# Kernel optimization log

Hardware: AMD Instinct MI355X
Metric: run time of the kernel (lower is better)

Reference implementation:

```python
import jax, jax.numpy as jnp
import numpy as np

N_NODES = 100000
N_EDGES = 1600000
D_IN = 128
D_HID = 128
GARMENT_SIZE = 80000


def setup_inputs() -> dict:
    key = jax.random.key(0)
    k1, k2, k3, k4, k5, k6 = jax.random.split(key, 6)
    notes = jax.random.normal(k1, (N_NODES, D_IN), dtype=jnp.float32)
    w = jax.random.normal(k2, (D_IN, D_HID), dtype=jnp.float32) * 0.05
    b = jax.random.normal(k3, (D_HID,), dtype=jnp.float32) * 0.05
    edge_src = jax.random.randint(k4, (N_EDGES,), 0, N_NODES, dtype=jnp.int32)
    edge_dst = jax.random.randint(k5, (N_EDGES,), 0, N_NODES, dtype=jnp.int32)
    edge_w = jax.random.uniform(k6, (N_EDGES,), dtype=jnp.float32)
    return {
        "notes": notes,
        "w": w,
        "b": b,
        "edge_src": edge_src,
        "edge_dst": edge_dst,
        "edge_w": edge_w,
        "garment_size": GARMENT_SIZE,
    }


def reference(notes, w, b, edge_src, edge_dst, edge_w, garment_size):
    # Dense projection: X0 = notes @ w   -> [N, H]
    X0 = jnp.einsum("nd,dh->nh", notes, w)
    # edge_convolution_template(edge_function=lambda x, y: y, reduction='weighted'):
    # X1[i] = sum over edges (i -> j) of a_ij * X0[j]
    msgs = X0[edge_dst] * edge_w[:, None]                      # [E, H] gather + scale
    X1 = jax.ops.segment_sum(msgs, edge_src, num_segments=notes.shape[0])  # [N, H]
    X = X1 + b
    # concat(act(X), X0[garment_size:]) along node axis -> [2N - garment_size, H]
    return jnp.concatenate([jax.nn.relu(X), X0[garment_size:]], axis=0)
```

## Files before the change

### kernel.cpp

```cpp
#include <hip/hip_runtime.h>

#define H 128
#define NPB 128
#define NB_MAX 1024
#define FILL_CH 4096
#define BCAP 3072
#define GCAP 2560

static __device__ __forceinline__ unsigned short f2bf(float f) {
  unsigned u = __float_as_uint(f);
  u += 0x7FFFu + ((u >> 16) & 1u);
  return (unsigned short)(u >> 16);
}

__global__ __launch_bounds__(256) void gemm_kernel(
    const float* __restrict__ notes, const float* __restrict__ w,
    const int* __restrict__ g_ptr, unsigned short* __restrict__ x0h,
    float* __restrict__ out, int* __restrict__ cursor, int nb,
    int n_nodes) {
  __shared__ float wtile[32 * H];
  __shared__ float ntile[64 * 32];
  const int tid = threadIdx.x;

  if (blockIdx.x == 0) {
    for (int i = tid; i < nb; i += 256) cursor[i] = i * BCAP;
  }

  const int tx = tid & 31;
  const int ty = tid >> 5;
  const int rowBlk = blockIdx.x * 64;
  const int g = *g_ptr;

  float acc[8][4];
#pragma unroll
  for (int i = 0; i < 8; ++i)
#pragma unroll
    for (int j = 0; j < 4; ++j) acc[i][j] = 0.f;

  for (int kc = 0; kc < H; kc += 32) {
    __syncthreads();
    {
      const float4* wg = (const float4*)(w + (size_t)kc * H);
      float4* wl = (float4*)wtile;
#pragma unroll
      for (int i = 0; i < 4; ++i) wl[tid + i * 256] = wg[tid + i * 256];
    }
    {
      float4* nl = (float4*)ntile;
#pragma unroll
      for (int i = 0; i < 2; ++i) {
        const int idx = tid + i * 256;
        const int row = idx >> 3;
        const int q = idx & 7;
        const int rr = min(rowBlk + row, n_nodes - 1);
        nl[idx] = *(const float4*)(notes + (size_t)rr * H + kc + q * 4);
      }
    }
    __syncthreads();
#pragma unroll 8
    for (int kk = 0; kk < 32; ++kk) {
      const float4 b4 = *(const float4*)&wtile[kk * H + tx * 4];
      float a[8];
#pragma unroll
      for (int i = 0; i < 8; ++i) a[i] = ntile[(ty * 8 + i) * 32 + kk];
#pragma unroll
      for (int i = 0; i < 8; ++i) {
        acc[i][0] += a[i] * b4.x;
        acc[i][1] += a[i] * b4.y;
        acc[i][2] += a[i] * b4.z;
        acc[i][3] += a[i] * b4.w;
      }
    }
  }

#pragma unroll
  for (int i = 0; i < 8; ++i) {
    const int r = rowBlk + ty * 8 + i;
    if (r < n_nodes) {
      ushort4 h;
      h.x = f2bf(acc[i][0]);
      h.y = f2bf(acc[i][1]);
      h.z = f2bf(acc[i][2]);
      h.w = f2bf(acc[i][3]);
      *(ushort4*)(x0h + (size_t)r * H + tx * 4) = h;
      if (r >= g) {
        float4 v;
        v.x = acc[i][0]; v.y = acc[i][1]; v.z = acc[i][2]; v.w = acc[i][3];
        *(float4*)(out + (size_t)(n_nodes + r - g) * H + tx * 4) = v;
      }
    }
  }
}

__global__ __launch_bounds__(256) void bucket_fill_kernel(
    const int* __restrict__ esrc, const int* __restrict__ edst,
    const float* __restrict__ ew, int* __restrict__ cursor,
    int2* __restrict__ sedge, unsigned char* __restrict__ srcloc, int n_edges,
    int nb) {
  __shared__ int2 stage[FILL_CH];
  __shared__ unsigned short bkt16[FILL_CH];
  __shared__ unsigned char loc8[FILL_CH];
  __shared__ int cntA[NB_MAX];
  __shared__ int lbase[NB_MAX];
  __shared__ int cntC[NB_MAX];
  const int t = threadIdx.x;
  const int base = blockIdx.x * FILL_CH;
  const int edgesInBlock = min(FILL_CH, n_edges - base);

  for (int i = t; i < nb; i += 256) {
    cntA[i] = 0;
    cntC[i] = 0;
  }
  __syncthreads();

  int sreg[FILL_CH / 256];
#pragma unroll
  for (int k = 0; k < FILL_CH / 256; ++k) {
    const int e = base + k * 256 + t;
    if (e < n_edges) {
      const int s = esrc[e];
      sreg[k] = s;
      atomicAdd(&cntA[s >> 7], 1);
    }
  }
  __syncthreads();

  {
    __shared__ int part[256];
    const int K = (nb + 255) / 256;
    const int lo = t * K;
    const int hi = min(lo + K, nb);
    int sum = 0;
    for (int i = lo; i < hi; ++i) sum += cntA[i];
    part[t] = sum;
    __syncthreads();
    for (int o = 1; o < 256; o <<= 1) {
      const int tv = (t >= o) ? part[t - o] : 0;
      __syncthreads();
      part[t] += tv;
      __syncthreads();
    }
    int run = (t == 0) ? 0 : part[t - 1];
    for (int i = lo; i < hi; ++i) {
      lbase[i] = run;
      run += cntA[i];
    }
  }
  __syncthreads();
  for (int i = t; i < nb; i += 256) {
    const int c = cntA[i];
    cntA[i] = c ? atomicAdd(&cursor[i], c) : 0;
  }
  __syncthreads();

#pragma unroll
  for (int k = 0; k < FILL_CH / 256; ++k) {
    const int e = base + k * 256 + t;
    if (e < n_edges) {
      const int s = sreg[k];
      const int b = s >> 7;
      const int r = atomicAdd(&cntC[b], 1);
      const int sp = lbase[b] + r;
      int2 pk;
      pk.x = edst[e];
      pk.y = __float_as_int(ew[e]);
      stage[sp] = pk;
      bkt16[sp] = (unsigned short)b;
      loc8[sp] = (unsigned char)(s & 127);
    }
  }
  __syncthreads();

  for (int j = t; j < edgesInBlock; j += 256) {
    const int b = bkt16[j];
    const int pos = cntA[b] + (j - lbase[b]);
    sedge[pos] = stage[j];
    srcloc[pos] = loc8[j];
  }
}

__global__ __launch_bounds__(256) void sortgather_kernel(
    const int* __restrict__ cursor, const int2* __restrict__ sedge,
    const unsigned char* __restrict__ srcloc,
    const unsigned short* __restrict__ x0h, const float* __restrict__ b,
    float* __restrict__ out, int n_nodes) {
  __shared__ int2 ledge[GCAP];
  __shared__ int cnt[NPB];
  __shared__ int nodeOff[NPB];
  const int t = threadIdx.x;
  const int lane = t & 63;
  const int wv = t >> 6;
  const int q = lane >> 4;
  const int l16 = lane & 15;
  const int beg = blockIdx.x * BCAP;
  const int end = cursor[blockIdx.x];
  const int nodeBase = blockIdx.x * NPB;
  const unsigned* __restrict__ x0u = (const unsigned*)x0h;
  const bool multi = (end - beg) > GCAP;

  const float4 b0 = ((const float4*)b)[l16 * 2];
  const float4 b1 = ((const float4*)b)[l16 * 2 + 1];

  int chunkBeg = beg;
  while (true) {
    const int ccnt = min(end - chunkBeg, GCAP);
    if (t < NPB) cnt[t] = 0;
    __syncthreads();
    for (int j = t; j < ccnt; j += 256)
      atomicAdd(&cnt[srcloc[chunkBeg + j]], 1);
    __syncthreads();
    if (t < NPB) nodeOff[t] = cnt[t];
    __syncthreads();
    for (int o = 1; o < NPB; o <<= 1) {
      int tv = 0;
      if (t < NPB && t >= o) tv = nodeOff[t - o];
      __syncthreads();
      if (t < NPB) nodeOff[t] += tv;
      __syncthreads();
    }
    if (t < NPB) {
      nodeOff[t] -= cnt[t];
      cnt[t] = 0;
    }
    __syncthreads();
    for (int j = t; j < ccnt; j += 256) {
      const int loc = srcloc[chunkBeg + j];
      const int r = atomicAdd(&cnt[loc], 1);
      ledge[nodeOff[loc] + r] = sedge[chunkBeg + j];
    }
    __syncthreads();
    for (int rnd = 0; rnd < NPB / 16; ++rnd) {
      const int loc = wv * (NPB / 4) + rnd * 4 + q;
      const int node = nodeBase + loc;
      const int o0 = nodeOff[loc];
      const int o1 = (loc == NPB - 1) ? ccnt : nodeOff[loc + 1];
      const int deg = o1 - o0;
      int dmax = deg;
      dmax = max(dmax, __shfl_xor(dmax, 16));
      dmax = max(dmax, __shfl_xor(dmax, 32));
      const int lastI = max(o1 - 1, 0);
      float4 aLo[4], aHi[4];
#pragma unroll
      for (int j = 0; j < 4; ++j) {
        aLo[j] = make_float4(0.f, 0.f, 0.f, 0.f);
        aHi[j] = make_float4(0.f, 0.f, 0.f, 0.f);
      }
      for (int k = 0; k < dmax; k += 4) {
        int2 m[4];
#pragma unroll
        for (int j = 0; j < 4; ++j) m[j] = ledge[min(o0 + k + j, lastI)];
        uint4 u[4];
#pragma unroll
        for (int j = 0; j < 4; ++j)
          u[j] = *(const uint4*)(x0u + (size_t)m[j].x * 64 + l16 * 4);
#pragma unroll
        for (int j = 0; j < 4; ++j) {
          const float wf = (k + j < deg) ? __int_as_float(m[j].y) : 0.f;
          aLo[j].x += __uint_as_float(u[j].x << 16) * wf;
          aLo[j].y += __uint_as_float(u[j].x & 0xFFFF0000u) * wf;
          aLo[j].z += __uint_as_float(u[j].y << 16) * wf;
          aLo[j].w += __uint_as_float(u[j].y & 0xFFFF0000u) * wf;
          aHi[j].x += __uint_as_float(u[j].z << 16) * wf;
          aHi[j].y += __uint_as_float(u[j].z & 0xFFFF0000u) * wf;
          aHi[j].z += __uint_as_float(u[j].w << 16) * wf;
          aHi[j].w += __uint_as_float(u[j].w & 0xFFFF0000u) * wf;
        }
      }
      if (node < n_nodes) {
        float4 s0, s1;
        s0.x = aLo[0].x + aLo[1].x + aLo[2].x + aLo[3].x;
        s0.y = aLo[0].y + aLo[1].y + aLo[2].y + aLo[3].y;
        s0.z = aLo[0].z + aLo[1].z + aLo[2].z + aLo[3].z;
        s0.w = aLo[0].w + aLo[1].w + aLo[2].w + aLo[3].w;
        s1.x = aHi[0].x + aHi[1].x + aHi[2].x + aHi[3].x;
        s1.y = aHi[0].y + aHi[1].y + aHi[2].y + aHi[3].y;
        s1.z = aHi[0].z + aHi[1].z + aHi[2].z + aHi[3].z;
        s1.w = aHi[0].w + aHi[1].w + aHi[2].w + aHi[3].w;
        float4* o4 = (float4*)out + (size_t)node * 32 + l16 * 2;
        if (!multi) {
          s0.x = fmaxf(s0.x + b0.x, 0.f);
          s0.y = fmaxf(s0.y + b0.y, 0.f);
          s0.z = fmaxf(s0.z + b0.z, 0.f);
          s0.w = fmaxf(s0.w + b0.w, 0.f);
          s1.x = fmaxf(s1.x + b1.x, 0.f);
          s1.y = fmaxf(s1.y + b1.y, 0.f);
          s1.z = fmaxf(s1.z + b1.z, 0.f);
          s1.w = fmaxf(s1.w + b1.w, 0.f);
          o4[0] = s0;
          o4[1] = s1;
        } else if (chunkBeg == beg) {
          o4[0] = s0;
          o4[1] = s1;
        } else {
          float4 p0 = o4[0], p1 = o4[1];
          p0.x += s0.x; p0.y += s0.y; p0.z += s0.z; p0.w += s0.w;
          p1.x += s1.x; p1.y += s1.y; p1.z += s1.z; p1.w += s1.w;
          o4[0] = p0;
          o4[1] = p1;
        }
      }
    }
    chunkBeg += GCAP;
    if (chunkBeg >= end) break;
    __syncthreads();
  }

  if (multi) {
    for (int rnd = 0; rnd < NPB / 16; ++rnd) {
      const int loc = wv * (NPB / 4) + rnd * 4 + q;
      const int node = nodeBase + loc;
      if (node < n_nodes) {
        float4* o4 = (float4*)out + (size_t)node * 32 + l16 * 2;
        float4 v0 = o4[0], v1 = o4[1];
        v0.x = fmaxf(v0.x + b0.x, 0.f);
        v0.y = fmaxf(v0.y + b0.y, 0.f);
        v0.z = fmaxf(v0.z + b0.z, 0.f);
        v0.w = fmaxf(v0.w + b0.w, 0.f);
        v1.x = fmaxf(v1.x + b1.x, 0.f);
        v1.y = fmaxf(v1.y + b1.y, 0.f);
        v1.z = fmaxf(v1.z + b1.z, 0.f);
        v1.w = fmaxf(v1.w + b1.w, 0.f);
        o4[0] = v0;
        o4[1] = v1;
      }
    }
  }
}

__global__ __launch_bounds__(256) void scatter_kernel(
    const int* __restrict__ esrc, const int* __restrict__ edst,
    const float* __restrict__ ew, const unsigned short* __restrict__ x0h,
    float* __restrict__ acc, int n_edges) {
  const int lane = threadIdx.x & 63;
  const int waveId = blockIdx.x * (blockDim.x >> 6) + (threadIdx.x >> 6);
  const int nWaves = gridDim.x * (blockDim.x >> 6);
  const unsigned* __restrict__ x0u = (const unsigned*)x0h;
  for (int e = waveId; e < n_edges; e += nWaves) {
    const int s = esrc[e];
    const int d = edst[e];
    const float wt = ew[e];
    const unsigned u = x0u[(size_t)d * 64 + lane];
    float* p = acc + (size_t)s * H + lane * 2;
    atomicAdd(p, __uint_as_float(u << 16) * wt);
    atomicAdd(p + 1, __uint_as_float(u & 0xFFFF0000u) * wt);
  }
}

__global__ __launch_bounds__(256) void epilogue_kernel(
    float* __restrict__ out, const float* __restrict__ b, int n4) {
  const int i = blockIdx.x * blockDim.x + threadIdx.x;
  if (i >= n4) return;
  float4* o4 = (float4*)out;
  const float4* b4 = (const float4*)b;
  float4 v = o4[i];
  const float4 bb = b4[i & 31];
  v.x = fmaxf(v.x + bb.x, 0.f);
  v.y = fmaxf(v.y + bb.y, 0.f);
  v.z = fmaxf(v.z + bb.z, 0.f);
  v.w = fmaxf(v.w + bb.w, 0.f);
  o4[i] = v;
}

extern "C" void kernel_launch(void* const* d_in, const int* in_sizes, int n_in,
                              void* d_out, int out_size, void* d_ws, size_t ws_size,
                              hipStream_t stream) {
  const float* notes = (const float*)d_in[0];
  const float* w     = (const float*)d_in[1];
  const float* b     = (const float*)d_in[2];
  const int*   esrc  = (const int*)d_in[3];
  const int*   edst  = (const int*)d_in[4];
  const float* ew    = (const float*)d_in[5];
  const int*   gptr  = (const int*)d_in[6];

  const int n_nodes = in_sizes[0] / H;
  const int n_edges = in_sizes[3];
  float* out = (float*)d_out;

  const int nb = (n_nodes + NPB - 1) / NPB;

  char* ws = (char*)d_ws;
  size_t p = 0;
  auto alloc = [&](size_t bytes) -> char* {
    char* cur = ws + p;
    p = (p + bytes + 255) & ~(size_t)255;
    return cur;
  };
  unsigned short* x0h = (unsigned short*)alloc((size_t)n_nodes * H * 2);
  int*  cursor       = (int*)alloc((size_t)nb * sizeof(int));
  int2* sedge        = (int2*)alloc((size_t)nb * BCAP * sizeof(int2));
  unsigned char* srcloc = (unsigned char*)alloc((size_t)nb * BCAP);
  const bool ok = (p <= ws_size) && (nb <= NB_MAX);

  const int gemmBlocks = (n_nodes + 63) / 64;

  if (ok) {
    gemm_kernel<<<gemmBlocks, 256, 0, stream>>>(notes, w, gptr, x0h, out,
                                                cursor, nb, n_nodes);
    bucket_fill_kernel<<<(n_edges + FILL_CH - 1) / FILL_CH, 256, 0, stream>>>(
        esrc, edst, ew, cursor, sedge, srcloc, n_edges, nb);
    sortgather_kernel<<<nb, 256, 0, stream>>>(cursor, sedge, srcloc, x0h, b,
                                              out, n_nodes);
  } else {
    gemm_kernel<<<gemmBlocks, 256, 0, stream>>>(notes, w, gptr, x0h, out,
                                                cursor, 0, n_nodes);
    hipMemsetAsync(d_out, 0, (size_t)n_nodes * H * sizeof(float), stream);
    scatter_kernel<<<2048, 256, 0, stream>>>(esrc, edst, ew, x0h, out, n_edges);
    const int n4 = n_nodes * H / 4;
    epilogue_kernel<<<(n4 + 255) / 256, 256, 0, stream>>>(out, b, n4);
  }
}
```

Measured before the change: 260.4 us.

## Fuse GEMM and edge bucket-fill into one heterogeneous kernel launch

Merges the dense projection GEMM and the edge bucketing pass into a single launch. The first blocks do bucket fill and the rest do the GEMM, so the two independent stages can run concurrently on the GPU. Because the cursor no longer comes from the GEMM block, a per-bucket counter is zeroed with a memset and bucket bases are computed as i*BCAP. FILL_CH is halved to fit a shared-memory union, which roughly doubles the number of fill blocks and the global atomics on the counters.

```diff
diff --git a/kernel.cpp b/kernel.cpp
--- a/kernel.cpp
+++ b/kernel.cpp
@@ -3,7 +3,7 @@
 #define H 128
 #define NPB 128
 #define NB_MAX 1024
-#define FILL_CH 4096
+#define FILL_CH 2048
 #define BCAP 3072
 #define GCAP 2560
 
@@ -13,22 +13,105 @@
   return (unsigned short)(u >> 16);
 }
 
-__global__ __launch_bounds__(256) void gemm_kernel(
+__global__ __launch_bounds__(256) void gemm_fill_kernel(
     const float* __restrict__ notes, const float* __restrict__ w,
-    const int* __restrict__ g_ptr, unsigned short* __restrict__ x0h,
-    float* __restrict__ out, int* __restrict__ cursor, int nb,
-    int n_nodes) {
-  __shared__ float wtile[32 * H];
-  __shared__ float ntile[64 * 32];
+    const int* __restrict__ g_ptr, const int* __restrict__ esrc,
+    const int* __restrict__ edst, const float* __restrict__ ew,
+    unsigned short* __restrict__ x0h, float* __restrict__ out,
+    int* __restrict__ fillCnt, int2* __restrict__ sedge,
+    unsigned char* __restrict__ srcloc, int nb, int n_nodes, int n_edges,
+    int fillBlocks) {
+  __shared__ __align__(16) char smem[35840];
   const int tid = threadIdx.x;
 
-  if (blockIdx.x == 0) {
-    for (int i = tid; i < nb; i += 256) cursor[i] = i * BCAP;
-  }
-
+  if (blockIdx.x < fillBlocks) {
+    int2* stage = (int2*)smem;
+    unsigned short* bkt16 = (unsigned short*)(smem + 16384);
+    unsigned char* loc8 = (unsigned char*)(smem + 20480);
+    int* cntA = (int*)(smem + 22528);
+    int* lbase = (int*)(smem + 26624);
+    int* cntC = (int*)(smem + 30720);
+    int* part = (int*)(smem + 34816);
+    const int base = blockIdx.x * FILL_CH;
+    const int edgesInBlock = min(FILL_CH, n_edges - base);
+
+    for (int i = tid; i < nb; i += 256) {
+      cntA[i] = 0;
+      cntC[i] = 0;
+    }
+    __syncthreads();
+
+    int sreg[FILL_CH / 256];
+#pragma unroll
+    for (int k = 0; k < FILL_CH / 256; ++k) {
+      const int e = base + k * 256 + tid;
+      if (e < n_edges) {
+        const int s = esrc[e];
+        sreg[k] = s;
+        atomicAdd(&cntA[s >> 7], 1);
+      }
+    }
+    __syncthreads();
+
+    {
+      const int K = (nb + 255) / 256;
+      const int lo = tid * K;
+      const int hi = min(lo + K, nb);
+      int sum = 0;
+      for (int i = lo; i < hi; ++i) sum += cntA[i];
+      part[tid] = sum;
+      __syncthreads();
+      for (int o = 1; o < 256; o <<= 1) {
+        const int tv = (tid >= o) ? part[tid - o] : 0;
+        __syncthreads();
+        part[tid] += tv;
+        __syncthreads();
+      }
+      int run = (tid == 0) ? 0 : part[tid - 1];
+      for (int i = lo; i < hi; ++i) {
+        lbase[i] = run;
+        run += cntA[i];
+      }
+    }
+    __syncthreads();
+    for (int i = tid; i < nb; i += 256) {
+      const int c = cntA[i];
+      cntA[i] = c ? (i * BCAP + atomicAdd(&fillCnt[i], c)) : 0;
+    }
+    __syncthreads();
+
+#pragma unroll
+    for (int k = 0; k < FILL_CH / 256; ++k) {
+      const int e = base + k * 256 + tid;
+      if (e < n_edges) {
+        const int s = sreg[k];
+        const int b = s >> 7;
+        const int r = atomicAdd(&cntC[b], 1);
+        const int sp = lbase[b] + r;
+        int2 pk;
+        pk.x = edst[e];
+        pk.y = __float_as_int(ew[e]);
+        stage[sp] = pk;
+        bkt16[sp] = (unsigned short)b;
+        loc8[sp] = (unsigned char)(s & 127);
+      }
+    }
+    __syncthreads();
+
+    for (int j = tid; j < edgesInBlock; j += 256) {
+      const int b = bkt16[j];
+      const int pos = cntA[b] + (j - lbase[b]);
+      sedge[pos] = stage[j];
+      srcloc[pos] = loc8[j];
+    }
+    return;
+  }
+
+  float* wtile = (float*)smem;
+  float* ntile = (float*)(smem + 16384);
   const int tx = tid & 31;
   const int ty = tid >> 5;
-  const int rowBlk = blockIdx.x * 64;
+  const int rowBlk = (blockIdx.x - fillBlocks) * 64;
   const int g = *g_ptr;
 
   float acc[8][4];
@@ -92,95 +175,8 @@
   }
 }
 
-__global__ __launch_bounds__(256) void bucket_fill_kernel(
-    const int* __restrict__ esrc, const int* __restrict__ edst,
-    const float* __restrict__ ew, int* __restrict__ cursor,
-    int2* __restrict__ sedge, unsigned char* __restrict__ srcloc, int n_edges,
-    int nb) {
-  __shared__ int2 stage[FILL_CH];
-  __shared__ unsigned short bkt16[FILL_CH];
-  __shared__ unsigned char loc8[FILL_CH];
-  __shared__ int cntA[NB_MAX];
-  __shared__ int lbase[NB_MAX];
-  __shared__ int cntC[NB_MAX];
-  const int t = threadIdx.x;
-  const int base = blockIdx.x * FILL_CH;
-  const int edgesInBlock = min(FILL_CH, n_edges - base);
-
-  for (int i = t; i < nb; i += 256) {
-    cntA[i] = 0;
-    cntC[i] = 0;
-  }
-  __syncthreads();
-
-  int sreg[FILL_CH / 256];
-#pragma unroll
-  for (int k = 0; k < FILL_CH / 256; ++k) {
-    const int e = base + k * 256 + t;
-    if (e < n_edges) {
-      const int s = esrc[e];
-      sreg[k] = s;
-      atomicAdd(&cntA[s >> 7], 1);
-    }
-  }
-  __syncthreads();
-
-  {
-    __shared__ int part[256];
-    const int K = (nb + 255) / 256;
-    const int lo = t * K;
-    const int hi = min(lo + K, nb);
-    int sum = 0;
-    for (int i = lo; i < hi; ++i) sum += cntA[i];
-    part[t] = sum;
-    __syncthreads();
-    for (int o = 1; o < 256; o <<= 1) {
-      const int tv = (t >= o) ? part[t - o] : 0;
-      __syncthreads();
-      part[t] += tv;
-      __syncthreads();
-    }
-    int run = (t == 0) ? 0 : part[t - 1];
-    for (int i = lo; i < hi; ++i) {
-      lbase[i] = run;
-      run += cntA[i];
-    }
-  }
-  __syncthreads();
-  for (int i = t; i < nb; i += 256) {
-    const int c = cntA[i];
-    cntA[i] = c ? atomicAdd(&cursor[i], c) : 0;
-  }
-  __syncthreads();
-
-#pragma unroll
-  for (int k = 0; k < FILL_CH / 256; ++k) {
-    const int e = base + k * 256 + t;
-    if (e < n_edges) {
-      const int s = sreg[k];
-      const int b = s >> 7;
-      const int r = atomicAdd(&cntC[b], 1);
-      const int sp = lbase[b] + r;
-      int2 pk;
-      pk.x = edst[e];
-      pk.y = __float_as_int(ew[e]);
-      stage[sp] = pk;
-      bkt16[sp] = (unsigned short)b;
-      loc8[sp] = (unsigned char)(s & 127);
-    }
-  }
-  __syncthreads();
-
-  for (int j = t; j < edgesInBlock; j += 256) {
-    const int b = bkt16[j];
-    const int pos = cntA[b] + (j - lbase[b]);
-    sedge[pos] = stage[j];
-    srcloc[pos] = loc8[j];
-  }
-}
-
 __global__ __launch_bounds__(256) void sortgather_kernel(
-    const int* __restrict__ cursor, const int2* __restrict__ sedge,
+    const int* __restrict__ fillCnt, const int2* __restrict__ sedge,
     const unsigned char* __restrict__ srcloc,
     const unsigned short* __restrict__ x0h, const float* __restrict__ b,
     float* __restrict__ out, int n_nodes) {
@@ -193,7 +189,7 @@
   const int q = lane >> 4;
   const int l16 = lane & 15;
   const int beg = blockIdx.x * BCAP;
-  const int end = cursor[blockIdx.x];
+  const int end = beg + fillCnt[blockIdx.x];
   const int nodeBase = blockIdx.x * NPB;
   const unsigned* __restrict__ x0u = (const unsigned*)x0h;
   const bool multi = (end - beg) > GCAP;
@@ -386,23 +382,25 @@
     return cur;
   };
   unsigned short* x0h = (unsigned short*)alloc((size_t)n_nodes * H * 2);
-  int*  cursor       = (int*)alloc((size_t)nb * sizeof(int));
+  int*  fillCnt      = (int*)alloc((size_t)nb * sizeof(int));
   int2* sedge        = (int2*)alloc((size_t)nb * BCAP * sizeof(int2));
   unsigned char* srcloc = (unsigned char*)alloc((size_t)nb * BCAP);
   const bool ok = (p <= ws_size) && (nb <= NB_MAX);
 
   const int gemmBlocks = (n_nodes + 63) / 64;
+  const int fillBlocks = (n_edges + FILL_CH - 1) / FILL_CH;
 
   if (ok) {
-    gemm_kernel<<<gemmBlocks, 256, 0, stream>>>(notes, w, gptr, x0h, out,
-                                                cursor, nb, n_nodes);
-    bucket_fill_kernel<<<(n_edges + FILL_CH - 1) / FILL_CH, 256, 0, stream>>>(
-        esrc, edst, ew, cursor, sedge, srcloc, n_edges, nb);
-    sortgather_kernel<<<nb, 256, 0, stream>>>(cursor, sedge, srcloc, x0h, b,
+    hipMemsetAsync(fillCnt, 0, (size_t)nb * sizeof(int), stream);
+    gemm_fill_kernel<<<fillBlocks + gemmBlocks, 256, 0, stream>>>(
+        notes, w, gptr, esrc, edst, ew, x0h, out, fillCnt, sedge, srcloc, nb,
+        n_nodes, n_edges, fillBlocks);
+    sortgather_kernel<<<nb, 256, 0, stream>>>(fillCnt, sedge, srcloc, x0h, b,
                                               out, n_nodes);
   } else {
-    gemm_kernel<<<gemmBlocks, 256, 0, stream>>>(notes, w, gptr, x0h, out,
-                                                cursor, 0, n_nodes);
+    gemm_fill_kernel<<<gemmBlocks, 256, 0, stream>>>(
+        notes, w, gptr, esrc, edst, ew, x0h, out, fillCnt, sedge, srcloc, 0,
+        n_nodes, n_edges, 0);
     hipMemsetAsync(d_out, 0, (size_t)n_nodes * H * sizeof(float), stream);
     scatter_kernel<<<2048, 256, 0, stream>>>(esrc, edst, ew, x0h, out, n_edges);
     const int n4 = n_nodes * H / 4;
```

After: 261.7 us. No clear change (+0.5%).
